# Kernel optimization log

Hardware: AMD Instinct MI355X
Metric: run time of the kernel (lower is better)

## Reference

```python
import jax, jax.numpy as jnp
import numpy as np

B, T, D = 4, 2048, 1024
DEPTH = 4
LEAF_DIM = 256
NUM_LEAVES = 2 ** DEPTH          # 16
NUM_NODES = NUM_LEAVES - 1       # 15


def _uniform(key, shape, scale):
    s = 1.0 / np.sqrt(scale)
    return jax.random.uniform(key, shape, minval=-s, maxval=s, dtype=jnp.float32)


def setup_inputs() -> dict:
    key = jax.random.key(0)
    ks = jax.random.split(key, 8)
    x = jax.random.normal(ks[0], (B, T, D), dtype=jnp.float32)
    # gate params: Dense(1) per internal node, level-order layout
    node_w = _uniform(ks[1], (NUM_NODES, D), D)
    node_b = _uniform(ks[2], (NUM_NODES,), D)
    # leaf MLP params: D -> LEAF_DIM -> D, stacked over leaves
    w1 = _uniform(ks[3], (NUM_LEAVES, D, LEAF_DIM), D)
    b1 = _uniform(ks[4], (NUM_LEAVES, LEAF_DIM), D)
    w2 = _uniform(ks[5], (NUM_LEAVES, LEAF_DIM, D), LEAF_DIM)
    b2 = _uniform(ks[6], (NUM_LEAVES, D), LEAF_DIM)
    return {"x": x, "node_w": node_w, "node_b": node_b,
            "w1": w1, "b1": b1, "w2": w2, "b2": b2, "training": 0}


def _leaf_probs(x, node_w, node_b, depth):
    # gate activations for all internal nodes at once: [B,T,NUM_NODES]
    c = jax.nn.sigmoid(jnp.einsum('btd,nd->btn', x, node_w) + node_b)
    probs = jnp.ones(c.shape[:-1] + (1,), dtype=c.dtype)
    for m in range(depth):
        start = 2 ** m - 1
        cl = c[..., start:start + 2 ** m]          # gates at level m: [B,T,2^m]
        # left child gets c, right child gets (1-c); interleave preserves
        # the recursion's n -> (2n, 2n+1) indexing
        probs = jnp.stack([probs * cl, probs * (1.0 - cl)], axis=-1)
        probs = probs.reshape(probs.shape[:-2] + (-1,))
    return probs                                   # [B,T,NUM_LEAVES]


def reference(x, node_w, node_b, w1, b1, w2, b2, training):
    num_leaves = w1.shape[0]
    depth = int(np.log2(num_leaves))
    probs = _leaf_probs(x, node_w, node_b, depth)          # [B,T,L]
    # all leaf MLP hidden layers as one batched GEMM
    h = jax.nn.relu(jnp.einsum('btd,ldh->btlh', x, w1) + b1)
    # weight hidden by leaf probability, then contract l and h together so the
    # [B,T,L,D] per-leaf output is never materialized
    h = h * probs[..., None]
    out = jnp.einsum('btlh,lhd->btd', h, w2)
    out = out + jnp.einsum('btl,ld->btd', probs, b2)
    return out
```

## Files before the change

kernel.cpp:

```cpp
#include <hip/hip_runtime.h>
#include <stdint.h>

typedef unsigned short ushort_t;
typedef __bf16 bf16x8 __attribute__((ext_vector_type(8)));
typedef float f32x4 __attribute__((ext_vector_type(4)));

#define M_TOK 8192
#define K1 1024
#define N1 4096
#define K2 4160
#define N2 1024

__device__ __forceinline__ ushort_t f2bf(float f) {
  union { float f; unsigned u; } v; v.f = f;
  unsigned u = v.u;
  u += 0x7FFFu + ((u >> 16) & 1u);
  return (ushort_t)(u >> 16);
}

__device__ __forceinline__ void gload16(const void* g, void* l) {
  __builtin_amdgcn_global_load_lds((__attribute__((address_space(1))) void*)g,
                                   (__attribute__((address_space(3))) void*)l,
                                   16, 0, 0);
}

__global__ __launch_bounds__(256) void k_probs(
    const float* __restrict__ x, const float* __restrict__ node_w,
    const float* __restrict__ node_b, ushort_t* __restrict__ xb,
    float* __restrict__ probs, ushort_t* __restrict__ hp) {
  const int wid = threadIdx.x >> 6, lane = threadIdx.x & 63;
  const int t = blockIdx.x * 4 + wid;
  const float* xr = x + (size_t)t * K1;
  float xv[16];
#pragma unroll
  for (int j = 0; j < 4; ++j) {
    float4 v = *(const float4*)(xr + j * 256 + lane * 4);
    xv[4*j+0] = v.x; xv[4*j+1] = v.y; xv[4*j+2] = v.z; xv[4*j+3] = v.w;
  }
  ushort_t* xbr = xb + (size_t)t * K1;
#pragma unroll
  for (int j = 0; j < 4; ++j) {
    ushort4 o;
    o.x = f2bf(xv[4*j+0]); o.y = f2bf(xv[4*j+1]);
    o.z = f2bf(xv[4*j+2]); o.w = f2bf(xv[4*j+3]);
    *(ushort4*)(xbr + j * 256 + lane * 4) = o;
  }
  float c[15];
#pragma unroll
  for (int n = 0; n < 15; ++n) {
    float s = 0.f;
    const float* wr = node_w + n * K1;
#pragma unroll
    for (int j = 0; j < 4; ++j) {
      float4 w = *(const float4*)(wr + j * 256 + lane * 4);
      s += xv[4*j+0]*w.x + xv[4*j+1]*w.y + xv[4*j+2]*w.z + xv[4*j+3]*w.w;
    }
#pragma unroll
    for (int off = 32; off > 0; off >>= 1) s += __shfl_xor(s, off);
    float z = s + node_b[n];
    c[n] = 1.f / (1.f + __expf(-z));
  }
  if (lane < 16) {
    float p = 1.f;
#pragma unroll
    for (int m = 0; m < 4; ++m) {
      int jm = lane >> (4 - m);
      int node = (1 << m) - 1 + jm;
      int bit = (lane >> (3 - m)) & 1;
      p *= bit ? (1.f - c[node]) : c[node];
    }
    probs[t * 16 + lane] = p;
    hp[(size_t)t * K2 + 4096 + lane] = f2bf(p);
  }
  if (lane < 48) hp[(size_t)t * K2 + 4112 + lane] = 0;
}

__global__ __launch_bounds__(256) void k_w1t(const float* __restrict__ w1,
                                             ushort_t* __restrict__ w1t) {
  __shared__ ushort_t tile[64][68];
  const int b = blockIdx.x;
  const int l = b >> 6, rem = b & 63;
  const int kt = rem >> 2, ht = rem & 3;
  const float* in = w1 + (size_t)l * K1 * 256;
  const int tr = threadIdx.x >> 4;
  const int tc = (threadIdx.x & 15) * 4;
#pragma unroll
  for (int rr = 0; rr < 4; ++rr) {
    int r = tr + rr * 16;
    float4 v = *(const float4*)(in + (size_t)(kt * 64 + r) * 256 + ht * 64 + tc);
    tile[r][tc+0] = f2bf(v.x); tile[r][tc+1] = f2bf(v.y);
    tile[r][tc+2] = f2bf(v.z); tile[r][tc+3] = f2bf(v.w);
  }
  __syncthreads();
#pragma unroll
  for (int rr = 0; rr < 4; ++rr) {
    int oh = tr + rr * 16;
    ushort4 o;
    o.x = tile[tc+0][oh]; o.y = tile[tc+1][oh];
    o.z = tile[tc+2][oh]; o.w = tile[tc+3][oh];
    *(ushort4*)(w1t + (size_t)(l * 256 + ht * 64 + oh) * K1 + kt * 64 + tc) = o;
  }
}

__global__ __launch_bounds__(256) void k_w2t(const float* __restrict__ w2,
                                             ushort_t* __restrict__ w2t) {
  __shared__ ushort_t tile[64][68];
  const int b = blockIdx.x;
  const int l = b >> 6, rem = b & 63;
  const int ht = rem >> 4, dt = rem & 15;
  const float* in = w2 + (size_t)l * 256 * N2;
  const int tr = threadIdx.x >> 4;
  const int tc = (threadIdx.x & 15) * 4;
#pragma unroll
  for (int rr = 0; rr < 4; ++rr) {
    int r = tr + rr * 16;
    float4 v = *(const float4*)(in + (size_t)(ht * 64 + r) * N2 + dt * 64 + tc);
    tile[r][tc+0] = f2bf(v.x); tile[r][tc+1] = f2bf(v.y);
    tile[r][tc+2] = f2bf(v.z); tile[r][tc+3] = f2bf(v.w);
  }
  __syncthreads();
#pragma unroll
  for (int rr = 0; rr < 4; ++rr) {
    int od = tr + rr * 16;
    ushort4 o;
    o.x = tile[tc+0][od]; o.y = tile[tc+1][od];
    o.z = tile[tc+2][od]; o.w = tile[tc+3][od];
    *(ushort4*)(w2t + (size_t)(dt * 64 + od) * K2 + l * 256 + ht * 64 + tc) = o;
  }
}

__global__ __launch_bounds__(256) void k_b2pad(const float* __restrict__ b2,
                                               ushort_t* __restrict__ w2t) {
  int tid = blockIdx.x * 256 + threadIdx.x;
  int d = tid >> 6, cc = tid & 63;
  float v = (cc < 16) ? b2[cc * N2 + d] : 0.f;
  w2t[(size_t)d * K2 + 4096 + cc] = f2bf(v);
}

template <int NT, int LDA, int LDB, int BN, int MODE>
__global__ __launch_bounds__(512, 2) void k_gemm8(
    const ushort_t* __restrict__ A, const ushort_t* __restrict__ Bt,
    const float* __restrict__ probs, const float* __restrict__ b1,
    ushort_t* __restrict__ hp, float* __restrict__ out, int ntn) {
  constexpr int BHR = BN / 2;
  constexpr int WN = (BN == 256) ? 4 : 2;
  constexpr int WM = 8 / WN;
  constexpr int FH = 128 / (WM * 16);
  constexpr int ABYTES = 128 * 128;
  constexpr int BBYTES = BHR * 128;
  constexpr int KEEP = 2 + 2 * (BHR / 64);

  extern __shared__ char lds[];
  const int tid = threadIdx.x;
  int bid = blockIdx.x;
  const int nwg = gridDim.x;
  bid = (bid & 7) * (nwg >> 3) + (bid >> 3);
  const int bm = bid / ntn, bn = bid % ntn;

  const int wid = tid >> 6, lane = tid & 63;
  const int widM = wid / WN, widN = wid % WN;
  const int wmBase = widM * (FH * 16);
  const int wn = widN * 64;
  const int lr = lane & 15, g = lane >> 4;

  const ushort_t* Ag = A + (size_t)bm * 256 * LDA;
  const ushort_t* Bg = Bt + (size_t)bn * BN * LDB;

  const int srow = tid >> 3;
  const int scol = ((tid & 7) << 4) ^ ((srow & 7) << 4);

  auto stageA = [&](int buf, int half, int kt) {
    const ushort_t* src = Ag + (size_t)(half * 128) * LDA + kt * 64;
    char* dst = lds + (buf * 2 + half) * ABYTES + tid * 16;
#pragma unroll
    for (int r = 0; r < 2; ++r)
      gload16((const char*)(src + (size_t)(srow + r * 64) * LDA) + scol,
              dst + r * 8192);
  };
  auto stageB = [&](int buf, int half, int kt) {
    const ushort_t* src = Bg + (size_t)(half * BHR) * LDB + kt * 64;
    char* dst = lds + 4 * ABYTES + (buf * 2 + half) * BBYTES + tid * 16;
#pragma unroll
    for (int r = 0; r < BHR / 64; ++r)
      gload16((const char*)(src + (size_t)(srow + r * 64) * LDB) + scol,
              dst + r * 8192);
  };
  auto rdA = [&](int buf, int half, int i, int kk) -> bf16x8 {
    int r = wmBase + i * 16 + lr;
    int off = r * 128 + (((kk * 4 + g) ^ (lr & 7)) << 4);
    return *(const bf16x8*)(lds + (buf * 2 + half) * ABYTES + off);
  };
  auto rdB = [&](int buf, int j, int kk) -> bf16x8 {
    int nr = wn + j * 16;
    int half = (nr >= BHR) ? 1 : 0;
    int r = (nr & (BHR - 1)) + lr;
    int off = r * 128 + (((kk * 4 + g) ^ (lr & 7)) << 4);
    return *(const bf16x8*)(lds + 4 * ABYTES + (buf * 2 + half) * BBYTES + off);
  };

  f32x4 acc[2 * FH][4];
#pragma unroll
  for (int i = 0; i < 2 * FH; ++i)
#pragma unroll
    for (int j = 0; j < 4; ++j) acc[i][j] = (f32x4){0.f, 0.f, 0.f, 0.f};

  stageA(0, 0, 0); stageA(0, 1, 0); stageB(0, 0, 0); stageB(0, 1, 0);
  stageA(1, 0, 1); stageB(1, 0, 1); stageB(1, 1, 1);
  {
    constexpr int kp = KEEP;
    if constexpr (kp == 6) asm volatile("s_waitcnt vmcnt(6)" ::: "memory");
    else                   asm volatile("s_waitcnt vmcnt(4)" ::: "memory");
  }
  __builtin_amdgcn_sched_barrier(0);
  __builtin_amdgcn_s_barrier();
  __builtin_amdgcn_sched_barrier(0);

#pragma unroll 1
  for (int kt = 0; kt < NT; ++kt) {
    const int cur = kt & 1;
    bf16x8 bfr[2][4];

    {
      bf16x8 a0[FH][2];
#pragma unroll
      for (int kk = 0; kk < 2; ++kk) {
#pragma unroll
        for (int i = 0; i < FH; ++i) a0[i][kk] = rdA(cur, 0, i, kk);
#pragma unroll
        for (int j = 0; j < 4; ++j) bfr[kk][j] = rdB(cur, j, kk);
      }
      if (kt + 1 < NT) stageA(cur ^ 1, 1, kt + 1);
      __builtin_amdgcn_s_setprio(1);
#pragma unroll
      for (int kk = 0; kk < 2; ++kk)
#pragma unroll
        for (int i = 0; i < FH; ++i)
#pragma unroll
          for (int j = 0; j < 4; ++j)
            acc[i][j] = __builtin_amdgcn_mfma_f32_16x16x32_bf16(
                a0[i][kk], bfr[kk][j], acc[i][j], 0, 0, 0);
      __builtin_amdgcn_s_setprio(0);
    }
    __builtin_amdgcn_s_barrier();
    __builtin_amdgcn_sched_barrier(0);

    {
      bf16x8 a1[FH][2];
#pragma unroll
      for (int kk = 0; kk < 2; ++kk)
#pragma unroll
        for (int i = 0; i < FH; ++i) a1[i][kk] = rdA(cur, 1, i, kk);
      if (kt + 2 < NT) {
        stageA(cur, 0, kt + 2);
        stageB(cur, 0, kt + 2);
        stageB(cur, 1, kt + 2);
      }
      __builtin_amdgcn_s_setprio(1);
#pragma unroll
      for (int kk = 0; kk < 2; ++kk)
#pragma unroll
        for (int i = 0; i < FH; ++i)
#pragma unroll
          for (int j = 0; j < 4; ++j)
            acc[FH + i][j] = __builtin_amdgcn_mfma_f32_16x16x32_bf16(
                a1[i][kk], bfr[kk][j], acc[FH + i][j], 0, 0, 0);
      __builtin_amdgcn_s_setprio(0);
    }
    if (kt + 2 < NT) {
      constexpr int kp = KEEP;
      if constexpr (kp == 6) asm volatile("s_waitcnt vmcnt(6)" ::: "memory");
      else                   asm volatile("s_waitcnt vmcnt(4)" ::: "memory");
      __builtin_amdgcn_sched_barrier(0);
    } else if (kt + 1 < NT) {
      asm volatile("s_waitcnt vmcnt(0)" ::: "memory");
      __builtin_amdgcn_sched_barrier(0);
    }
    __builtin_amdgcn_s_barrier();
    __builtin_amdgcn_sched_barrier(0);
  }

  const int rowb = bm * 256 + wmBase + g * 4;
  const int colb = bn * BN + wn + lr;
  if (MODE == 0) {
    const int leaf = bn;
#pragma unroll
    for (int q = 0; q < 2; ++q)
#pragma unroll
      for (int i = 0; i < FH; ++i) {
        int rbase = rowb + q * 128 + i * 16;
        float pm[4];
#pragma unroll
        for (int rg = 0; rg < 4; ++rg)
          pm[rg] = probs[(size_t)(rbase + rg) * 16 + leaf];
#pragma unroll
        for (int j = 0; j < 4; ++j) {
          float bias = b1[colb + j * 16];
#pragma unroll
          for (int rg = 0; rg < 4; ++rg) {
            float v = acc[q * FH + i][j][rg] + bias;
            v = v > 0.f ? v : 0.f;
            v *= pm[rg];
            hp[(size_t)(rbase + rg) * K2 + colb + j * 16] = f2bf(v);
          }
        }
      }
  } else {
#pragma unroll
    for (int q = 0; q < 2; ++q)
#pragma unroll
      for (int i = 0; i < FH; ++i) {
        int rbase = rowb + q * 128 + i * 16;
#pragma unroll
        for (int j = 0; j < 4; ++j)
#pragma unroll
          for (int rg = 0; rg < 4; ++rg)
            out[(size_t)(rbase + rg) * N2 + colb + j * 16] = acc[q * FH + i][j][rg];
      }
  }
}

extern "C" void kernel_launch(void* const* d_in, const int* in_sizes, int n_in,
                              void* d_out, int out_size, void* d_ws, size_t ws_size,
                              hipStream_t stream) {
  const float* x      = (const float*)d_in[0];
  const float* node_w = (const float*)d_in[1];
  const float* node_b = (const float*)d_in[2];
  const float* w1     = (const float*)d_in[3];
  const float* b1     = (const float*)d_in[4];
  const float* w2     = (const float*)d_in[5];
  const float* b2     = (const float*)d_in[6];
  float* out = (float*)d_out;

  char* ws = (char*)d_ws;
  ushort_t* xb    = (ushort_t*)(ws);
  ushort_t* w1t   = (ushort_t*)(ws + 16777216);
  ushort_t* w2t   = (ushort_t*)(ws + 25165824);
  ushort_t* hp    = (ushort_t*)(ws + 33685504);
  float*    probs = (float*)   (ws + 101842944);

  k_probs<<<M_TOK / 4, 256, 0, stream>>>(x, node_w, node_b, xb, probs, hp);
  k_w1t<<<1024, 256, 0, stream>>>(w1, w1t);
  k_w2t<<<1024, 256, 0, stream>>>(w2, w2t);
  k_b2pad<<<256, 256, 0, stream>>>(b2, w2t);
  k_gemm8<16, K1, K1, 256, 0><<<512, 512, 131072, stream>>>(
      xb, w1t, probs, b1, hp, nullptr, N1 / 256);
  k_gemm8<65, K2, K2, 128, 1><<<256, 512, 98304, stream>>>(
      hp, w2t, nullptr, nullptr, nullptr, out, N2 / 128);
}
```

Baseline: 184.2 us.

## Merge weight-prep kernels and interleave LDS reads with MFMAs via sched groups

Combines the three weight transpose/convert kernels (w1, w2, b2 padding) into a single launch with block-index dispatch, which removes two kernel launch gaps. In both GEMM main-loop halves it reorders the MFMA loops to iterate j outer, i inner, and adds sched_group_barrier hints so LDS reads are interleaved with MFMA groups rather than issued all up front. This is meant to hide LDS latency behind matrix work. The scheduling hints depend on the compiler honoring the group counts and could also constrain scheduling in a way that hurts.

Result: faster. 179.3 us (-2.6%).

```diff
diff --git a/kernel.cpp b/kernel.cpp
--- a/kernel.cpp
+++ b/kernel.cpp
@@ -10,6 +10,10 @@
 #define N1 4096
 #define K2 4160
 #define N2 1024
+
+#define SGB(m, n) __builtin_amdgcn_sched_group_barrier((m), (n), 0)
+#define SGB_DS   0x100
+#define SGB_MFMA 0x008
 
 __device__ __forceinline__ ushort_t f2bf(float f) {
   union { float f; unsigned u; } v; v.f = f;
@@ -75,66 +79,61 @@
   if (lane < 48) hp[(size_t)t * K2 + 4112 + lane] = 0;
 }
 
-__global__ __launch_bounds__(256) void k_w1t(const float* __restrict__ w1,
-                                             ushort_t* __restrict__ w1t) {
+__global__ __launch_bounds__(256) void k_wprep(
+    const float* __restrict__ w1, const float* __restrict__ w2,
+    const float* __restrict__ b2, ushort_t* __restrict__ w1t,
+    ushort_t* __restrict__ w2t) {
   __shared__ ushort_t tile[64][68];
   const int b = blockIdx.x;
-  const int l = b >> 6, rem = b & 63;
-  const int kt = rem >> 2, ht = rem & 3;
-  const float* in = w1 + (size_t)l * K1 * 256;
   const int tr = threadIdx.x >> 4;
   const int tc = (threadIdx.x & 15) * 4;
-#pragma unroll
-  for (int rr = 0; rr < 4; ++rr) {
-    int r = tr + rr * 16;
-    float4 v = *(const float4*)(in + (size_t)(kt * 64 + r) * 256 + ht * 64 + tc);
-    tile[r][tc+0] = f2bf(v.x); tile[r][tc+1] = f2bf(v.y);
-    tile[r][tc+2] = f2bf(v.z); tile[r][tc+3] = f2bf(v.w);
-  }
-  __syncthreads();
-#pragma unroll
-  for (int rr = 0; rr < 4; ++rr) {
-    int oh = tr + rr * 16;
-    ushort4 o;
-    o.x = tile[tc+0][oh]; o.y = tile[tc+1][oh];
-    o.z = tile[tc+2][oh]; o.w = tile[tc+3][oh];
-    *(ushort4*)(w1t + (size_t)(l * 256 + ht * 64 + oh) * K1 + kt * 64 + tc) = o;
-  }
-}
-
-__global__ __launch_bounds__(256) void k_w2t(const float* __restrict__ w2,
-                                             ushort_t* __restrict__ w2t) {
-  __shared__ ushort_t tile[64][68];
-  const int b = blockIdx.x;
-  const int l = b >> 6, rem = b & 63;
-  const int ht = rem >> 4, dt = rem & 15;
-  const float* in = w2 + (size_t)l * 256 * N2;
-  const int tr = threadIdx.x >> 4;
-  const int tc = (threadIdx.x & 15) * 4;
-#pragma unroll
-  for (int rr = 0; rr < 4; ++rr) {
-    int r = tr + rr * 16;
-    float4 v = *(const float4*)(in + (size_t)(ht * 64 + r) * N2 + dt * 64 + tc);
-    tile[r][tc+0] = f2bf(v.x); tile[r][tc+1] = f2bf(v.y);
-    tile[r][tc+2] = f2bf(v.z); tile[r][tc+3] = f2bf(v.w);
-  }
-  __syncthreads();
-#pragma unroll
-  for (int rr = 0; rr < 4; ++rr) {
-    int od = tr + rr * 16;
-    ushort4 o;
-    o.x = tile[tc+0][od]; o.y = tile[tc+1][od];
-    o.z = tile[tc+2][od]; o.w = tile[tc+3][od];
-    *(ushort4*)(w2t + (size_t)(dt * 64 + od) * K2 + l * 256 + ht * 64 + tc) = o;
-  }
-}
-
-__global__ __launch_bounds__(256) void k_b2pad(const float* __restrict__ b2,
-                                               ushort_t* __restrict__ w2t) {
-  int tid = blockIdx.x * 256 + threadIdx.x;
-  int d = tid >> 6, cc = tid & 63;
-  float v = (cc < 16) ? b2[cc * N2 + d] : 0.f;
-  w2t[(size_t)d * K2 + 4096 + cc] = f2bf(v);
+  if (b < 1024) {
+    const int l = b >> 6, rem = b & 63;
+    const int kt = rem >> 2, ht = rem & 3;
+    const float* in = w1 + (size_t)l * K1 * 256;
+#pragma unroll
+    for (int rr = 0; rr < 4; ++rr) {
+      int r = tr + rr * 16;
+      float4 v = *(const float4*)(in + (size_t)(kt * 64 + r) * 256 + ht * 64 + tc);
+      tile[r][tc+0] = f2bf(v.x); tile[r][tc+1] = f2bf(v.y);
+      tile[r][tc+2] = f2bf(v.z); tile[r][tc+3] = f2bf(v.w);
+    }
+    __syncthreads();
+#pragma unroll
+    for (int rr = 0; rr < 4; ++rr) {
+      int oh = tr + rr * 16;
+      ushort4 o;
+      o.x = tile[tc+0][oh]; o.y = tile[tc+1][oh];
+      o.z = tile[tc+2][oh]; o.w = tile[tc+3][oh];
+      *(ushort4*)(w1t + (size_t)(l * 256 + ht * 64 + oh) * K1 + kt * 64 + tc) = o;
+    }
+  } else if (b < 2048) {
+    const int bb = b - 1024;
+    const int l = bb >> 6, rem = bb & 63;
+    const int ht = rem >> 4, dt = rem & 15;
+    const float* in = w2 + (size_t)l * 256 * N2;
+#pragma unroll
+    for (int rr = 0; rr < 4; ++rr) {
+      int r = tr + rr * 16;
+      float4 v = *(const float4*)(in + (size_t)(ht * 64 + r) * N2 + dt * 64 + tc);
+      tile[r][tc+0] = f2bf(v.x); tile[r][tc+1] = f2bf(v.y);
+      tile[r][tc+2] = f2bf(v.z); tile[r][tc+3] = f2bf(v.w);
+    }
+    __syncthreads();
+#pragma unroll
+    for (int rr = 0; rr < 4; ++rr) {
+      int od = tr + rr * 16;
+      ushort4 o;
+      o.x = tile[tc+0][od]; o.y = tile[tc+1][od];
+      o.z = tile[tc+2][od]; o.w = tile[tc+3][od];
+      *(ushort4*)(w2t + (size_t)(dt * 64 + od) * K2 + l * 256 + ht * 64 + tc) = o;
+    }
+  } else {
+    int tid = (b - 2048) * 256 + threadIdx.x;
+    int d = tid >> 6, cc = tid & 63;
+    float v = (cc < 16) ? b2[cc * N2 + d] : 0.f;
+    w2t[(size_t)d * K2 + 4096 + cc] = f2bf(v);
+  }
 }
 
 template <int NT, int LDA, int LDB, int BN, int MODE>
@@ -206,11 +205,8 @@
 
   stageA(0, 0, 0); stageA(0, 1, 0); stageB(0, 0, 0); stageB(0, 1, 0);
   stageA(1, 0, 1); stageB(1, 0, 1); stageB(1, 1, 1);
-  {
-    constexpr int kp = KEEP;
-    if constexpr (kp == 6) asm volatile("s_waitcnt vmcnt(6)" ::: "memory");
-    else                   asm volatile("s_waitcnt vmcnt(4)" ::: "memory");
-  }
+  if constexpr (KEEP == 6) asm volatile("s_waitcnt vmcnt(6)" ::: "memory");
+  else                     asm volatile("s_waitcnt vmcnt(4)" ::: "memory");
   __builtin_amdgcn_sched_barrier(0);
   __builtin_amdgcn_s_barrier();
   __builtin_amdgcn_sched_barrier(0);
@@ -234,12 +230,18 @@
 #pragma unroll
       for (int kk = 0; kk < 2; ++kk)
 #pragma unroll
-        for (int i = 0; i < FH; ++i)
-#pragma unroll
-          for (int j = 0; j < 4; ++j)
+        for (int j = 0; j < 4; ++j)
+#pragma unroll
+          for (int i = 0; i < FH; ++i)
             acc[i][j] = __builtin_amdgcn_mfma_f32_16x16x32_bf16(
                 a0[i][kk], bfr[kk][j], acc[i][j], 0, 0, 0);
       __builtin_amdgcn_s_setprio(0);
+#pragma unroll
+      for (int kk = 0; kk < 2; ++kk) {
+        SGB(SGB_DS, FH + 1); SGB(SGB_MFMA, FH);
+#pragma unroll
+        for (int rep = 0; rep < 3; ++rep) { SGB(SGB_DS, 1); SGB(SGB_MFMA, FH); }
+      }
     }
     __builtin_amdgcn_s_barrier();
     __builtin_amdgcn_sched_barrier(0);
@@ -259,17 +261,20 @@
 #pragma unroll
       for (int kk = 0; kk < 2; ++kk)
 #pragma unroll
-        for (int i = 0; i < FH; ++i)
-#pragma unroll
-          for (int j = 0; j < 4; ++j)
+        for (int j = 0; j < 4; ++j)
+#pragma unroll
+          for (int i = 0; i < FH; ++i)
             acc[FH + i][j] = __builtin_amdgcn_mfma_f32_16x16x32_bf16(
                 a1[i][kk], bfr[kk][j], acc[FH + i][j], 0, 0, 0);
       __builtin_amdgcn_s_setprio(0);
+#pragma unroll
+      for (int kk = 0; kk < 2; ++kk) {
+        SGB(SGB_DS, FH); SGB(SGB_MFMA, 2 * FH); SGB(SGB_MFMA, 2 * FH);
+      }
     }
     if (kt + 2 < NT) {
-      constexpr int kp = KEEP;
-      if constexpr (kp == 6) asm volatile("s_waitcnt vmcnt(6)" ::: "memory");
-      else                   asm volatile("s_waitcnt vmcnt(4)" ::: "memory");
+      if constexpr (KEEP == 6) asm volatile("s_waitcnt vmcnt(6)" ::: "memory");
+      else                     asm volatile("s_waitcnt vmcnt(4)" ::: "memory");
       __builtin_amdgcn_sched_barrier(0);
     } else if (kt + 1 < NT) {
       asm volatile("s_waitcnt vmcnt(0)" ::: "memory");
@@ -339,9 +344,7 @@
   float*    probs = (float*)   (ws + 101842944);
 
   k_probs<<<M_TOK / 4, 256, 0, stream>>>(x, node_w, node_b, xb, probs, hp);
-  k_w1t<<<1024, 256, 0, stream>>>(w1, w1t);
-  k_w2t<<<1024, 256, 0, stream>>>(w2, w2t);
-  k_b2pad<<<256, 256, 0, stream>>>(b2, w2t);
+  k_wprep<<<2304, 256, 0, stream>>>(w1, w2, b2, w1t, w2t);
   k_gemm8<16, K1, K1, 256, 0><<<512, 512, 131072, stream>>>(
       xb, w1t, probs, b1, hp, nullptr, N1 / 256);
   k_gemm8<65, K2, K2, 128, 1><<<256, 512, 98304, stream>>>(
```
